# Optimization experiments

Measured on AMD Instinct MI355X. Metric: run time of the kernel, lower is better.

Reference implementation:

```python
import jax, jax.numpy as jnp
import numpy as np

B, C, H, W = 32, 3, 224, 224
P = 16                 # patch size
D = 768                # embed_size
NH = 12                # num heads
HD = D // NH           # head size
L = 12                 # depth
MLP = 4 * D
NC = 1000              # num classes
GH, GW = H // P, W // P
T = GH * GW            # tokens = 196
PATCH_DIM = P * P * C
EPS = 1e-5


def posemb_sincos_2d(h, w, dim, temperature=10000.0):
    yy, xx = jnp.meshgrid(jnp.arange(h, dtype=jnp.float32),
                          jnp.arange(w, dtype=jnp.float32), indexing='ij')
    omega = jnp.arange(dim // 4, dtype=jnp.float32) / (dim // 4 - 1)
    omega = 1.0 / (temperature ** omega)
    yv = yy.reshape(-1)[:, None] * omega[None, :]
    xv = xx.reshape(-1)[:, None] * omega[None, :]
    return jnp.concatenate([jnp.sin(xv), jnp.cos(xv), jnp.sin(yv), jnp.cos(yv)], axis=1)


def layernorm(x, g, b):
    mu = jnp.mean(x, axis=-1, keepdims=True)
    var = jnp.mean((x - mu) ** 2, axis=-1, keepdims=True)
    return (x - mu) * jax.lax.rsqrt(var + EPS) * g + b


def setup_inputs() -> dict:
    key = jax.random.key(0)
    ks = jax.random.split(key, 16)
    s = 0.02
    inp = {
        'x': jax.random.normal(ks[0], (B, C, H, W), jnp.float32),
        'embed_W': jax.random.normal(ks[1], (PATCH_DIM, D), jnp.float32) * s,
        'embed_b': jnp.zeros((D,), jnp.float32),
        'Wq': jax.random.normal(ks[2], (L, NH, D, HD), jnp.float32) * s,
        'Wk': jax.random.normal(ks[3], (L, NH, D, HD), jnp.float32) * s,
        'Wv': jax.random.normal(ks[4], (L, NH, D, HD), jnp.float32) * s,
        'Wo': jax.random.normal(ks[5], (L, D, D), jnp.float32) * s,
        'bo': jnp.zeros((L, D), jnp.float32),
        'ln1_g': jnp.ones((L, D), jnp.float32),
        'ln1_b': jnp.zeros((L, D), jnp.float32),
        'ln2_g': jnp.ones((L, D), jnp.float32),
        'ln2_b': jnp.zeros((L, D), jnp.float32),
        'W1': jax.random.normal(ks[6], (L, D, MLP), jnp.float32) * s,
        'b1': jnp.zeros((L, MLP), jnp.float32),
        'W2': jax.random.normal(ks[7], (L, MLP, D), jnp.float32) * s,
        'b2': jnp.zeros((L, D), jnp.float32),
        'head_W': jax.random.normal(ks[8], (D, NC), jnp.float32) * s,
    }
    return inp


def reference(x, embed_W, embed_b, Wq, Wk, Wv, Wo, bo,
              ln1_g, ln1_b, ln2_g, ln2_b, W1, b1, W2, b2, head_W):
    # patchify: b c (h p1) (w p2) -> b (h w) (p1 p2 c)
    p = x.reshape(B, C, GH, P, GW, P)
    p = p.transpose(0, 2, 4, 3, 5, 1).reshape(B, T, PATCH_DIM)
    h = p @ embed_W + embed_b + posemb_sincos_2d(GH, GW, D)[None]  # [B,T,D]

    scale = HD ** -0.5
    for l in range(L):
        xn = layernorm(h, ln1_g[l], ln1_b[l])
        q = jnp.einsum('btd,hde->bhte', xn, Wq[l])
        k = jnp.einsum('btd,hde->bhte', xn, Wk[l])
        v = jnp.einsum('btd,hde->bhte', xn, Wv[l])
        scores = jax.nn.softmax(jnp.einsum('bhte,bhse->bhts', q, k) * scale, axis=-1)
        att = jnp.einsum('bhts,bhse->bhte', scores, v)
        att = att.transpose(0, 2, 1, 3).reshape(B, T, D)  # concat heads
        h = h + att @ Wo[l] + bo[l]
        xn = layernorm(h, ln2_g[l], ln2_b[l])
        h = h + jax.nn.gelu(xn @ W1[l] + b1[l], approximate=False) @ W2[l] + b2[l]

    return h.mean(axis=1) @ head_W  # [B, NC]
```

## Files before the change

kernel.cpp:

```cpp
#include <hip/hip_runtime.h>
#include <cstdint>


typedef __bf16 bf16_t;
typedef __bf16 bf16x8 __attribute__((ext_vector_type(8)));
typedef __bf16 bf16x4 __attribute__((ext_vector_type(4)));
typedef float  f32x4  __attribute__((ext_vector_type(4)));

#define NLAYER 12
#define BMPAD 56
#define PSTRIDE 4816896l

__device__ __forceinline__ void g2lds16(const void* g, void* l) {
  __builtin_amdgcn_global_load_lds(
      (const __attribute__((address_space(1))) void*)g,
      (__attribute__((address_space(3))) void*)l, 16, 0, 0);
}

__global__ __launch_bounds__(256) void tcvt(
    const float* __restrict__ in, bf16_t* __restrict__ out,
    int R, int C, long inStride, long outOuter, long outInner, int innerN)
{
  int bi = blockIdx.z;
  in  += (long)bi * inStride;
  out += (long)(bi / innerN) * outOuter + (long)(bi % innerN) * outInner;
  __shared__ float t[32][33];
  int c0 = blockIdx.x * 32, r0 = blockIdx.y * 32;
  int tx = threadIdx.x, ty = threadIdx.y;
  #pragma unroll
  for (int i = ty; i < 32; i += 8) {
    int r = r0 + i, c = c0 + tx;
    if (r < R && c < C) t[i][tx] = in[(long)r * C + c];
  }
  __syncthreads();
  #pragma unroll
  for (int i = ty; i < 32; i += 8) {
    int c = c0 + i, r = r0 + tx;
    if (r < R && c < C) out[(long)c * R + r] = (bf16_t)t[tx][i];
  }
}

__global__ __launch_bounds__(256) void patchify(
    const float* __restrict__ x, bf16_t* __restrict__ patches)
{
  int idx = blockIdx.x * 256 + threadIdx.x;
  int bt = idx / 768, pd = idx % 768;
  int b = bt / 196, t = bt % 196;
  int gh = t / 14, gw = t % 14;
  int p1 = pd / 48, rem = pd % 48;
  int p2 = rem / 3, c = rem % 3;
  float v = x[(((long)(b * 3 + c) * 224) + gh * 16 + p1) * 224 + gw * 16 + p2];
  patches[idx] = (bf16_t)v;
}

__global__ __launch_bounds__(256) void hinit(
    const float* __restrict__ eb, float* __restrict__ h)
{
  int idx = blockIdx.x * 256 + threadIdx.x;
  int t = idx / 768, d = idx % 768;
  int gh = t / 14, gw = t % 14;
  int quadrant = d / 192, i = d % 192;
  float omega = powf(10000.0f, -(float)i / 191.0f);
  float arg = (quadrant < 2 ? (float)gw : (float)gh) * omega;
  float pv = ((quadrant & 1) == 0) ? sinf(arg) : cosf(arg);
  float v = pv + eb[d];
  #pragma unroll
  for (int b = 0; b < 32; ++b) h[(long)b * 150528 + idx] = v;
}

__global__ __launch_bounds__(256) void ln_fuse(
    float* __restrict__ h, const bf16_t* __restrict__ pbuf, int nparts,
    const float* __restrict__ bias, const float* __restrict__ g,
    const float* __restrict__ bb, bf16_t* __restrict__ xn)
{
  int row = blockIdx.x * 4 + (threadIdx.x >> 6);
  int lane = threadIdx.x & 63;
  float* hr = h + (long)row * 768;
  const bf16_t* pr = pbuf + (long)row * 768;
  float4 v[3];
  float s = 0.f, s2 = 0.f;
  #pragma unroll
  for (int i = 0; i < 3; ++i) {
    int c4 = lane + 64 * i;
    float4 hv = ((const float4*)hr)[c4];
    float4 acc = {0.f, 0.f, 0.f, 0.f};
    for (int pp = 0; pp < nparts; ++pp) {
      bf16x4 q = *(const bf16x4*)(pr + (long)pp * PSTRIDE + c4 * 4);
      acc.x += (float)q[0]; acc.y += (float)q[1];
      acc.z += (float)q[2]; acc.w += (float)q[3];
    }
    if (bias) {
      float4 bv = ((const float4*)bias)[c4];
      acc.x += bv.x; acc.y += bv.y; acc.z += bv.z; acc.w += bv.w;
    }
    hv.x += acc.x; hv.y += acc.y; hv.z += acc.z; hv.w += acc.w;
    ((float4*)hr)[c4] = hv;
    v[i] = hv;
    s  += hv.x + hv.y + hv.z + hv.w;
    s2 += hv.x * hv.x + hv.y * hv.y + hv.z * hv.z + hv.w * hv.w;
  }
  #pragma unroll
  for (int d = 1; d < 64; d <<= 1) {
    s  += __shfl_xor(s, d, 64);
    s2 += __shfl_xor(s2, d, 64);
  }
  float mu = s * (1.0f / 768.0f);
  float var = s2 * (1.0f / 768.0f) - mu * mu;
  float rs = rsqrtf(var + 1e-5f);
  uint2* outv = (uint2*)(xn + (long)row * 768);
  const float4* gv = (const float4*)g;
  const float4* bv2 = (const float4*)bb;
  #pragma unroll
  for (int i = 0; i < 3; ++i) {
    int c4 = lane + 64 * i;
    float4 gg = gv[c4], b4 = bv2[c4];
    union { bf16_t q[4]; uint2 u; } pk;
    pk.q[0] = (bf16_t)((v[i].x - mu) * rs * gg.x + b4.x);
    pk.q[1] = (bf16_t)((v[i].y - mu) * rs * gg.y + b4.y);
    pk.q[2] = (bf16_t)((v[i].z - mu) * rs * gg.z + b4.z);
    pk.q[3] = (bf16_t)((v[i].w - mu) * rs * gg.w + b4.w);
    outv[c4] = pk.u;
  }
}

__device__ __forceinline__ float gelu_fast(float x) {
  float y = 0.7978845608f * (x + 0.044715f * x * x * x);
  float e = __expf(2.0f * y);
  float t = 1.0f - 2.0f / (e + 1.0f);
  return 0.5f * x * (1.0f + t);
}

template <int EPI, int KTOT, int KS>
__global__ __launch_bounds__(256, 4) void gemm_bt(
    const bf16_t* __restrict__ A, const bf16_t* __restrict__ Bt,
    int ldc, int Mstore, int Nstore,
    const float* __restrict__ bias,
    float* __restrict__ fout, bf16_t* __restrict__ bout)
{
  int lin = blockIdx.x;
  int bm = lin % BMPAD;
  if (bm * 128 >= Mstore) return;
  int rest = lin / BMPAD;
  int ks = rest % KS;
  int bn = rest / KS;
  constexpr int Ksl = KTOT / KS;
  int k0 = ks * Ksl;

  __shared__ __align__(16) bf16_t As[128 * 64];
  __shared__ __align__(16) bf16_t Bs[128 * 64];
  int tid = threadIdx.x;
  int wave = tid >> 6, lane = tid & 63, quad = lane >> 4, l16 = lane & 15;
  int wm = wave >> 1, wn = wave & 1;
  const bf16_t* Ab = A + (long)bm * 128 * KTOT;
  const bf16_t* Bb = Bt + (long)bn * 128 * KTOT;

  f32x4 zero = {0.f, 0.f, 0.f, 0.f};
  f32x4 acc[4][4];
  #pragma unroll
  for (int i = 0; i < 4; ++i)
    #pragma unroll
    for (int j = 0; j < 4; ++j) acc[i][j] = zero;

  int srow = tid >> 3;
  int sgcol = ((tid & 7) ^ (srow & 7)) * 8;
  int ldst = tid * 16;

  int aoff[2][4], boff[2][4];
  #pragma unroll
  for (int kh = 0; kh < 2; ++kh)
    #pragma unroll
    for (int i = 0; i < 4; ++i) {
      int ra = wm * 64 + i * 16 + l16;
      int rb = wn * 64 + i * 16 + l16;
      int pa = ((kh * 4 + quad) ^ (ra & 7)) * 8;
      int pb = ((kh * 4 + quad) ^ (rb & 7)) * 8;
      aoff[kh][i] = ra * 64 + pa;
      boff[kh][i] = rb * 64 + pb;
    }

  for (int kt = k0; kt < k0 + Ksl; kt += 64) {
    __syncthreads();
    #pragma unroll
    for (int c = 0; c < 4; ++c) {
      g2lds16(Ab + (long)(c * 32 + srow) * KTOT + kt + sgcol,
              (char*)As + c * 4096 + ldst);
      g2lds16(Bb + (long)(c * 32 + srow) * KTOT + kt + sgcol,
              (char*)Bs + c * 4096 + ldst);
    }
    __syncthreads();

    #pragma unroll
    for (int kh = 0; kh < 2; ++kh) {
      bf16x8 af[4], bfr[4];
      #pragma unroll
      for (int i = 0; i < 4; ++i) af[i] = *(const bf16x8*)(As + aoff[kh][i]);
      #pragma unroll
      for (int j = 0; j < 4; ++j) bfr[j] = *(const bf16x8*)(Bs + boff[kh][j]);
      #pragma unroll
      for (int i = 0; i < 4; ++i)
        #pragma unroll
        for (int j = 0; j < 4; ++j)
          acc[i][j] = __builtin_amdgcn_mfma_f32_16x16x32_bf16(af[i], bfr[j], acc[i][j], 0, 0, 0);
    }
  }

  int m0 = bm * 128 + wm * 64, n0 = bn * 128 + wn * 64;
  #pragma unroll
  for (int i = 0; i < 4; ++i)
    #pragma unroll
    for (int j = 0; j < 4; ++j)
      #pragma unroll
      for (int r = 0; r < 4; ++r) {
        int row = m0 + i * 16 + quad * 4 + r;
        int col = n0 + j * 16 + l16;
        if (row >= Mstore || col >= Nstore) continue;
        float v = acc[i][j][r];
        if (EPI == 0) {
          bout[(long)row * ldc + col] = (bf16_t)v;
        } else if (EPI == 3) {
          bout[(long)row * ldc + col] = (bf16_t)gelu_fast(v + bias[col]);
        } else if (EPI == 4) {
          fout[(long)row * ldc + col] = v;
        } else {
          bout[(long)ks * PSTRIDE + (long)row * ldc + col] = (bf16_t)v;
        }
      }
}

__global__ __launch_bounds__(256) void vtrans(
    const bf16_t* __restrict__ qkv, bf16_t* __restrict__ Vt)
{
  int bh = blockIdx.z, b = bh / 12, h = bh % 12;
  __shared__ bf16_t t[32][33];
  int e0 = blockIdx.x * 32, s0 = blockIdx.y * 32;
  int tx = threadIdx.x, ty = threadIdx.y;
  #pragma unroll
  for (int i = ty; i < 32; i += 8) {
    int s = s0 + i;
    bf16_t v = (bf16_t)0.0f;
    if (s < 196) v = qkv[(long)(b * 196 + s) * 2304 + 1536 + h * 64 + e0 + tx];
    t[i][tx] = v;
  }
  __syncthreads();
  #pragma unroll
  for (int i = ty; i < 32; i += 8) {
    int e = e0 + i, s = s0 + tx;
    if (s < 224) Vt[(long)bh * 64 * 224 + (long)e * 224 + s] = t[tx][i];
  }
}

__global__ __launch_bounds__(64) void attn_fused(
    const bf16_t* __restrict__ qkv, const bf16_t* __restrict__ Vt,
    bf16_t* __restrict__ att)
{
  __shared__ __align__(16) bf16_t Pl[16 * 232];
  int mt = blockIdx.x, bh = blockIdx.y;
  int b = bh / 12, h = bh % 12;
  int lane = threadIdx.x, quad = lane >> 4, l16 = lane & 15;

  #pragma unroll
  for (int i = 0; i < 4; ++i) {
    int idx = lane + 64 * i;
    Pl[(idx >> 4) * 232 + 208 + (idx & 15)] = (bf16_t)0.0f;
  }

  f32x4 zero = {0.f, 0.f, 0.f, 0.f};
  f32x4 acc[13];
  #pragma unroll
  for (int nt = 0; nt < 13; ++nt) acc[nt] = zero;

  long qoff = (long)(b * 196 + mt * 16 + l16) * 2304 + h * 64;
  #pragma unroll
  for (int kk = 0; kk < 2; ++kk) {
    bf16x8 a = *(const bf16x8*)(qkv + qoff + kk * 32 + quad * 8);
    #pragma unroll
    for (int nt = 0; nt < 13; ++nt) {
      long koff = (long)(b * 196 + nt * 16 + l16) * 2304 + 768 + h * 64 + kk * 32 + quad * 8;
      bf16x8 bb = *(const bf16x8*)(qkv + koff);
      acc[nt] = __builtin_amdgcn_mfma_f32_16x16x32_bf16(a, bb, acc[nt], 0, 0, 0);
    }
  }

  float p[13][4];
  #pragma unroll
  for (int nt = 0; nt < 13; ++nt)
    #pragma unroll
    for (int r = 0; r < 4; ++r) {
      float v = acc[nt][r] * 0.125f;
      if (nt == 12 && l16 >= 4) v = -1e30f;
      p[nt][r] = v;
    }

  #pragma unroll
  for (int r = 0; r < 4; ++r) {
    float mx = -1e30f;
    #pragma unroll
    for (int nt = 0; nt < 13; ++nt) mx = fmaxf(mx, p[nt][r]);
    #pragma unroll
    for (int d = 1; d < 16; d <<= 1) mx = fmaxf(mx, __shfl_xor(mx, d, 64));
    float sm = 0.f;
    #pragma unroll
    for (int nt = 0; nt < 13; ++nt) {
      float e = __expf(p[nt][r] - mx);
      p[nt][r] = e;
      sm += e;
    }
    #pragma unroll
    for (int d = 1; d < 16; d <<= 1) sm += __shfl_xor(sm, d, 64);
    float inv = 1.0f / sm;
    #pragma unroll
    for (int nt = 0; nt < 13; ++nt) p[nt][r] *= inv;
  }

  #pragma unroll
  for (int nt = 0; nt < 13; ++nt)
    #pragma unroll
    for (int r = 0; r < 4; ++r)
      Pl[(quad * 4 + r) * 232 + nt * 16 + l16] = (bf16_t)p[nt][r];
  __syncthreads();

  f32x4 pv[4];
  #pragma unroll
  for (int nt = 0; nt < 4; ++nt) pv[nt] = zero;
  const bf16_t* Vb = Vt + (long)bh * 64 * 224;
  #pragma unroll
  for (int ks = 0; ks < 7; ++ks) {
    bf16x8 a = *(const bf16x8*)(Pl + l16 * 232 + ks * 32 + quad * 8);
    #pragma unroll
    for (int nt = 0; nt < 4; ++nt) {
      bf16x8 bb = *(const bf16x8*)(Vb + (long)(nt * 16 + l16) * 224 + ks * 32 + quad * 8);
      pv[nt] = __builtin_amdgcn_mfma_f32_16x16x32_bf16(a, bb, pv[nt], 0, 0, 0);
    }
  }

  #pragma unroll
  for (int nt = 0; nt < 4; ++nt)
    #pragma unroll
    for (int r = 0; r < 4; ++r) {
      int t = mt * 16 + quad * 4 + r;
      if (t < 196)
        att[(long)(b * 196 + t) * 768 + h * 64 + nt * 16 + l16] = (bf16_t)pv[nt][r];
    }
}

__global__ __launch_bounds__(256) void meanpool_fuse(
    const float* __restrict__ h, const bf16_t* __restrict__ pbuf,
    const float* __restrict__ bias, bf16_t* __restrict__ hm)
{
  int d = blockIdx.y * 256 + threadIdx.x;
  int b = blockIdx.x;
  float s = 0.f;
  for (int t = 0; t < 196; ++t) {
    long idx = (long)(b * 196 + t) * 768 + d;
    float v = h[idx];
    #pragma unroll
    for (int pp = 0; pp < 4; ++pp) v += (float)pbuf[idx + pp * PSTRIDE];
    s += v;
  }
  hm[b * 768 + d] = (bf16_t)(s * (1.0f / 196.0f) + bias[d]);
}

extern "C" void kernel_launch(void* const* d_in, const int* in_sizes, int n_in,
                              void* d_out, int out_size, void* d_ws, size_t ws_size,
                              hipStream_t stream)
{
  const float* x       = (const float*)d_in[0];
  const float* embed_W = (const float*)d_in[1];
  const float* embed_b = (const float*)d_in[2];
  const float* Wq      = (const float*)d_in[3];
  const float* Wk      = (const float*)d_in[4];
  const float* Wv      = (const float*)d_in[5];
  const float* Wo      = (const float*)d_in[6];
  const float* bo      = (const float*)d_in[7];
  const float* ln1_g   = (const float*)d_in[8];
  const float* ln1_b   = (const float*)d_in[9];
  const float* ln2_g   = (const float*)d_in[10];
  const float* ln2_b   = (const float*)d_in[11];
  const float* W1      = (const float*)d_in[12];
  const float* b1      = (const float*)d_in[13];
  const float* W2      = (const float*)d_in[14];
  const float* b2      = (const float*)d_in[15];
  const float* head_W  = (const float*)d_in[16];

  char* p = (char*)d_ws;
  auto carve = [&](size_t bytes) {
    char* r = p;
    p += (bytes + 255) & ~(size_t)255;
    return r;
  };
  bf16_t* embed_Wt = (bf16_t*)carve(589824ull * 2);
  bf16_t* qkvT     = (bf16_t*)carve(21233664ull * 2);
  bf16_t* WoT      = (bf16_t*)carve(7077888ull * 2);
  bf16_t* W1T      = (bf16_t*)carve(28311552ull * 2);
  bf16_t* W2T      = (bf16_t*)carve(28311552ull * 2);
  bf16_t* headWt   = (bf16_t*)carve(786432ull * 2);
  bf16_t* patches  = (bf16_t*)carve(4816896ull * 2);
  float*  h        = (float*)carve(4816896ull * 4);
  bf16_t* xn       = (bf16_t*)carve(4816896ull * 2);
  bf16_t* qkv      = (bf16_t*)carve(14487552ull * 2);
  bf16_t* Vt       = (bf16_t*)carve(5505024ull * 2);
  bf16_t* hmlp     = (bf16_t*)carve(19267584ull * 2);
  bf16_t* att      = (bf16_t*)carve(4816896ull * 2);
  bf16_t* pbuf     = (bf16_t*)carve(4ull * PSTRIDE * 2);
  bf16_t* hm       = (bf16_t*)carve(98304ull * 2);
  (void)ws_size; (void)n_in; (void)in_sizes; (void)out_size;

  dim3 tb32(32, 8);

  tcvt<<<dim3(24, 24, 1),   tb32, 0, stream>>>(embed_W, embed_Wt, 768, 768, 0, 0, 0, 1);
  tcvt<<<dim3(24, 24, 12),  tb32, 0, stream>>>(Wo, WoT, 768, 768, 589824, 589824, 0, 1);
  tcvt<<<dim3(2, 24, 144),  tb32, 0, stream>>>(Wq, qkvT,           768, 64, 49152, 1769472, 49152, 12);
  tcvt<<<dim3(2, 24, 144),  tb32, 0, stream>>>(Wk, qkvT + 589824,  768, 64, 49152, 1769472, 49152, 12);
  tcvt<<<dim3(2, 24, 144),  tb32, 0, stream>>>(Wv, qkvT + 1179648, 768, 64, 49152, 1769472, 49152, 12);
  tcvt<<<dim3(96, 24, 12),  tb32, 0, stream>>>(W1, W1T, 768, 3072, 2359296, 2359296, 0, 1);
  tcvt<<<dim3(24, 96, 12),  tb32, 0, stream>>>(W2, W2T, 3072, 768, 2359296, 2359296, 0, 1);
  tcvt<<<dim3(32, 24, 1),   tb32, 0, stream>>>(head_W, headWt, 768, 1000, 0, 0, 0, 1);

  patchify<<<18816, 256, 0, stream>>>(x, patches);
  hinit<<<588, 256, 0, stream>>>(embed_b, h);

  gemm_bt<5, 768, 2><<<BMPAD * 6 * 2, 256, 0, stream>>>(
      patches, embed_Wt, 768, 6272, 768, nullptr, nullptr, pbuf);

  for (int l = 0; l < NLAYER; ++l) {
    ln_fuse<<<1568, 256, 0, stream>>>(
        h, pbuf, l == 0 ? 2 : 4, l == 0 ? nullptr : b2 + (l - 1) * 768,
        ln1_g + l * 768, ln1_b + l * 768, xn);
    gemm_bt<0, 768, 1><<<BMPAD * 18, 256, 0, stream>>>(
        xn, qkvT + (long)l * 1769472, 2304, 6272, 2304,
        nullptr, nullptr, qkv);
    vtrans<<<dim3(2, 7, 384), tb32, 0, stream>>>(qkv, Vt);
    attn_fused<<<dim3(13, 384), 64, 0, stream>>>(qkv, Vt, att);
    gemm_bt<5, 768, 2><<<BMPAD * 6 * 2, 256, 0, stream>>>(
        att, WoT + (long)l * 589824, 768, 6272, 768,
        nullptr, nullptr, pbuf);
    ln_fuse<<<1568, 256, 0, stream>>>(
        h, pbuf, 2, bo + l * 768, ln2_g + l * 768, ln2_b + l * 768, xn);
    gemm_bt<3, 768, 1><<<BMPAD * 24, 256, 0, stream>>>(
        xn, W1T + (long)l * 2359296, 3072, 6272, 3072,
        b1 + l * 3072, nullptr, hmlp);
    gemm_bt<5, 3072, 4><<<BMPAD * 6 * 4, 256, 0, stream>>>(
        hmlp, W2T + (long)l * 2359296, 768, 6272, 768,
        nullptr, nullptr, pbuf);
  }

  meanpool_fuse<<<dim3(32, 3), 256, 0, stream>>>(h, pbuf, b2 + 11 * 768, hm);
  gemm_bt<4, 768, 1><<<BMPAD * 8, 256, 0, stream>>>(
      hm, headWt, 1000, 32, 1000, nullptr, (float*)d_out, nullptr);
}
```

Measured before the change: 3.247 ms.

## Add 256x256 double-buffered GEMM kernel for QKV and MLP projections

Introduces a new 512-thread GEMM with 256x256 output tiles, swizzled LDS layout, direct global-to-LDS loads and an interleaved staging/compute pipeline with explicit waitcnt and barriers. The QKV, MLP-up (with GELU) and MLP-down projections now use it, and the down projection's split-K changes from 4 to 3 slices, with ln_fuse and meanpool updated to sum three partial buffers. The aim is more reuse per tile and better overlap of loads with MFMA work on the largest GEMMs. In exchange it uses larger shared memory per block, and the row padding to 6400 adds wasted tile work.

Result: slower. 3.522 ms (+8.5%).

```diff
diff --git a/kernel.cpp b/kernel.cpp
--- a/kernel.cpp
+++ b/kernel.cpp
@@ -10,6 +10,7 @@
 #define NLAYER 12
 #define BMPAD 56
 #define PSTRIDE 4816896l
+#define NBM256 25
 
 __device__ __forceinline__ void g2lds16(const void* g, void* l) {
   __builtin_amdgcn_global_load_lds(
@@ -215,14 +216,141 @@
         int col = n0 + j * 16 + l16;
         if (row >= Mstore || col >= Nstore) continue;
         float v = acc[i][j][r];
-        if (EPI == 0) {
-          bout[(long)row * ldc + col] = (bf16_t)v;
-        } else if (EPI == 3) {
-          bout[(long)row * ldc + col] = (bf16_t)gelu_fast(v + bias[col]);
-        } else if (EPI == 4) {
+        if (EPI == 4) {
           fout[(long)row * ldc + col] = v;
         } else {
           bout[(long)ks * PSTRIDE + (long)row * ldc + col] = (bf16_t)v;
+        }
+      }
+}
+
+#define VMW(N)                                                     \
+  do {                                                             \
+    asm volatile("s_waitcnt vmcnt(" #N ")" ::: "memory");          \
+    __builtin_amdgcn_sched_barrier(0);                             \
+  } while (0)
+
+#define STAGEH(G, L, BUF, H, KT)                                              \
+  do {                                                                        \
+    g2lds16((G) + (long)((H) * 128 + srow) * KTOT + (KT) + scol,              \
+            (char*)(L) + (BUF) * 32768 + (H) * 16384 + ldst);                 \
+    g2lds16((G) + (long)((H) * 128 + 64 + srow) * KTOT + (KT) + scol,         \
+            (char*)(L) + (BUF) * 32768 + (H) * 16384 + 8192 + ldst);          \
+  } while (0)
+
+#define COMPUTE(Q, BUF, STAGEOP, TAILOP)                                      \
+  do {                                                                        \
+    const char* Ap_ = (const char*)As + (BUF) * 32768 + abase + (Q) * 4096;   \
+    const char* Bp_ = (const char*)Bs + (BUF) * 32768 + bbase;                \
+    bf16x8 af[2][2];                                                          \
+    _Pragma("unroll") for (int ii = 0; ii < 2; ++ii)                          \
+      _Pragma("unroll") for (int kh = 0; kh < 2; ++kh)                        \
+        af[ii][kh] = *(const bf16x8*)(Ap_ + ii * 2048 + pgo[kh]);             \
+    if ((Q) == 0) {                                                           \
+      _Pragma("unroll") for (int j = 0; j < 4; ++j)                           \
+        _Pragma("unroll") for (int kh = 0; kh < 2; ++kh)                      \
+          bfr[j][kh] = *(const bf16x8*)(Bp_ + j * 2048 + pgo[kh]);            \
+    }                                                                         \
+    STAGEOP;                                                                  \
+    __builtin_amdgcn_s_barrier();                                             \
+    asm volatile("s_waitcnt lgkmcnt(0)" ::: "memory");                        \
+    __builtin_amdgcn_s_setprio(1);                                            \
+    _Pragma("unroll") for (int kh = 0; kh < 2; ++kh)                          \
+      _Pragma("unroll") for (int ii = 0; ii < 2; ++ii)                        \
+        _Pragma("unroll") for (int j = 0; j < 4; ++j)                         \
+          acc[2 * (Q) + ii][j] = __builtin_amdgcn_mfma_f32_16x16x32_bf16(     \
+              af[ii][kh], bfr[j][kh], acc[2 * (Q) + ii][j], 0, 0, 0);         \
+    __builtin_amdgcn_s_setprio(0);                                            \
+    TAILOP;                                                                   \
+    __builtin_amdgcn_s_barrier();                                             \
+  } while (0)
+
+template <int EPI, int KTOT, int KS>
+__global__ __launch_bounds__(512, 2) void gemm256(
+    const bf16_t* __restrict__ A, const bf16_t* __restrict__ Bt,
+    int ldc, int Mstore, const float* __restrict__ bias,
+    bf16_t* __restrict__ bout)
+{
+  constexpr int Ksl = KTOT / KS;
+  constexpr int NI  = Ksl / 128;
+  int lin = blockIdx.x;
+  int bm = lin % NBM256;
+  int rest = lin / NBM256;
+  int ks = rest % KS;
+  int bn = rest / KS;
+  int k0 = ks * Ksl;
+
+  __shared__ __align__(16) bf16_t As[2][256 * 64];
+  __shared__ __align__(16) bf16_t Bs[2][256 * 64];
+
+  int tid = threadIdx.x;
+  int lane = tid & 63, wave = tid >> 6;
+  int quad = lane >> 4, l16 = lane & 15;
+  int wm = wave >> 2, wn = wave & 3;
+
+  const bf16_t* Ab = A + (long)bm * 256 * KTOT;
+  const bf16_t* Bb = Bt + (long)bn * 256 * KTOT;
+
+  int srow = tid >> 3;
+  int scol = ((tid & 7) ^ (srow & 7)) * 8;
+  int ldst = tid * 16;
+
+  int pgo[2];
+  pgo[0] = ((0 * 4 + quad) ^ (l16 & 7)) * 16;
+  pgo[1] = ((1 * 4 + quad) ^ (l16 & 7)) * 16;
+  int abase = (wm * 128 + l16) * 128;
+  int bbase = (wn * 64 + l16) * 128;
+
+  f32x4 acc[8][4];
+  f32x4 zero = {0.f, 0.f, 0.f, 0.f};
+  #pragma unroll
+  for (int i = 0; i < 8; ++i)
+    #pragma unroll
+    for (int j = 0; j < 4; ++j) acc[i][j] = zero;
+  bf16x8 bfr[4][2];
+
+  STAGEH(Ab, As, 0, 0, k0);
+  STAGEH(Ab, As, 0, 1, k0);
+  STAGEH(Bb, Bs, 0, 0, k0);
+  STAGEH(Bb, Bs, 0, 1, k0);
+  STAGEH(Bb, Bs, 1, 0, k0 + 64);
+  STAGEH(Bb, Bs, 1, 1, k0 + 64);
+  VMW(4);
+  __builtin_amdgcn_s_barrier();
+
+  #pragma unroll 1
+  for (int i = 0; i < NI; ++i) {
+    int kb = k0 + i * 128;
+    bool nl = (i + 1 < NI);
+    COMPUTE(0, 0, STAGEH(Ab, As, 1, 0, kb + 64), (void)0);
+    COMPUTE(1, 0, STAGEH(Ab, As, 1, 1, kb + 64), (void)0);
+    COMPUTE(2, 0, { if (nl) STAGEH(Bb, Bs, 0, 0, kb + 128); }, (void)0);
+    COMPUTE(3, 0, { if (nl) STAGEH(Bb, Bs, 0, 1, kb + 128); },
+            { if (nl) VMW(4); else VMW(0); });
+    COMPUTE(0, 1, { if (nl) STAGEH(Ab, As, 0, 0, kb + 128); }, (void)0);
+    COMPUTE(1, 1, { if (nl) STAGEH(Ab, As, 0, 1, kb + 128); }, (void)0);
+    COMPUTE(2, 1, { if (nl) STAGEH(Bb, Bs, 1, 0, kb + 192); }, (void)0);
+    COMPUTE(3, 1, { if (nl) STAGEH(Bb, Bs, 1, 1, kb + 192); },
+            { if (nl) VMW(4); });
+  }
+
+  int m0 = bm * 256 + wm * 128, n0 = bn * 256 + wn * 64;
+  #pragma unroll
+  for (int i = 0; i < 8; ++i)
+    #pragma unroll
+    for (int j = 0; j < 4; ++j)
+      #pragma unroll
+      for (int r = 0; r < 4; ++r) {
+        int row = m0 + i * 16 + quad * 4 + r;
+        if (row >= Mstore) continue;
+        int col = n0 + j * 16 + l16;
+        float v = acc[i][j][r];
+        if (EPI == 3) {
+          bout[(long)row * ldc + col] = (bf16_t)gelu_fast(v + bias[col]);
+        } else if (EPI == 5) {
+          bout[(long)ks * PSTRIDE + (long)row * ldc + col] = (bf16_t)v;
+        } else {
+          bout[(long)row * ldc + col] = (bf16_t)v;
         }
       }
 }
@@ -354,7 +482,7 @@
     long idx = (long)(b * 196 + t) * 768 + d;
     float v = h[idx];
     #pragma unroll
-    for (int pp = 0; pp < 4; ++pp) v += (float)pbuf[idx + pp * PSTRIDE];
+    for (int pp = 0; pp < 3; ++pp) v += (float)pbuf[idx + pp * PSTRIDE];
     s += v;
   }
   hm[b * 768 + d] = (bf16_t)(s * (1.0f / 196.0f) + bias[d]);
@@ -424,11 +552,10 @@
 
   for (int l = 0; l < NLAYER; ++l) {
     ln_fuse<<<1568, 256, 0, stream>>>(
-        h, pbuf, l == 0 ? 2 : 4, l == 0 ? nullptr : b2 + (l - 1) * 768,
+        h, pbuf, l == 0 ? 2 : 3, l == 0 ? nullptr : b2 + (l - 1) * 768,
         ln1_g + l * 768, ln1_b + l * 768, xn);
-    gemm_bt<0, 768, 1><<<BMPAD * 18, 256, 0, stream>>>(
-        xn, qkvT + (long)l * 1769472, 2304, 6272, 2304,
-        nullptr, nullptr, qkv);
+    gemm256<0, 768, 1><<<NBM256 * 9, 512, 0, stream>>>(
+        xn, qkvT + (long)l * 1769472, 2304, 6272, nullptr, qkv);
     vtrans<<<dim3(2, 7, 384), tb32, 0, stream>>>(qkv, Vt);
     attn_fused<<<dim3(13, 384), 64, 0, stream>>>(qkv, Vt, att);
     gemm_bt<5, 768, 2><<<BMPAD * 6 * 2, 256, 0, stream>>>(
@@ -436,12 +563,10 @@
         nullptr, nullptr, pbuf);
     ln_fuse<<<1568, 256, 0, stream>>>(
         h, pbuf, 2, bo + l * 768, ln2_g + l * 768, ln2_b + l * 768, xn);
-    gemm_bt<3, 768, 1><<<BMPAD * 24, 256, 0, stream>>>(
-        xn, W1T + (long)l * 2359296, 3072, 6272, 3072,
-        b1 + l * 3072, nullptr, hmlp);
-    gemm_bt<5, 3072, 4><<<BMPAD * 6 * 4, 256, 0, stream>>>(
-        hmlp, W2T + (long)l * 2359296, 768, 6272, 768,
-        nullptr, nullptr, pbuf);
+    gemm256<3, 768, 1><<<NBM256 * 12, 512, 0, stream>>>(
+        xn, W1T + (long)l * 2359296, 3072, 6272, b1 + l * 3072, hmlp);
+    gemm256<5, 3072, 3><<<NBM256 * 3 * 3, 512, 0, stream>>>(
+        hmlp, W2T + (long)l * 2359296, 768, 6272, nullptr, pbuf);
   }
 
   meanpool_fuse<<<dim3(32, 3), 256, 0, stream>>>(h, pbuf, b2 + 11 * 768, hm);
```
